# Kernel tuning notes

Hardware: AMD Instinct MI355X
Metric: run time of the kernel (lower is better)

The kernel has to match this reference:

```python
import jax, jax.numpy as jnp
import numpy as np

IN_FEATURES = 4096
OUT_FEATURES = 4096
SHARED_ROWS = 512
BATCH = 4096


def setup_inputs() -> dict:
    key = jax.random.key(0)
    k1, k2, k3 = jax.random.split(key, 3)
    x = jax.random.normal(k1, (BATCH, IN_FEATURES), dtype=jnp.float32)
    shared_weights = jax.random.normal(k2, (SHARED_ROWS, IN_FEATURES), dtype=jnp.float32)
    bias = jax.random.normal(k3, (OUT_FEATURES,), dtype=jnp.float32)
    return {"x": x, "shared_weights": shared_weights, "bias": bias}


def reference(x, shared_weights, bias):
    # Original: W = shared_weights.repeat(out_features // shared_rows, 1)  -> [out, in]
    #           y = x @ W.T + bias
    # Row i of W equals shared_weights[i % shared_rows], so the output columns are a
    # tile of the small GEMM result — compute the small GEMM once and tile (same math,
    # avoids materializing the full [out, in] weight).
    reps = OUT_FEATURES // SHARED_ROWS
    y_small = jnp.einsum("bi,ri->br", x, shared_weights)  # [batch, shared_rows]
    y = jnp.tile(y_small, (1, reps)) + bias  # [batch, out_features]
    return y
```

## Files before the change

### kernel.cpp

```cpp
#include <hip/hip_runtime.h>
#include <hip/hip_bf16.h>


typedef __bf16 bf8 __attribute__((ext_vector_type(8)));
typedef float f4 __attribute__((ext_vector_type(4)));
typedef unsigned int uint;

constexpr int M = 4096;
constexpr int K = 4096;
constexpr int NS = 512;
constexpr int OUTF = 4096;
constexpr int BM = 128, BN = 128, BK = 32;
constexpr int SK = 4;
constexpr int KS = K / SK;
constexpr int NITER = KS / BK;

#define PERM_HI2(hi, lo) __builtin_amdgcn_perm((hi), (lo), 0x07060302u)

__device__ __forceinline__ void async16(const float* g, float* l) {
  __builtin_amdgcn_global_load_lds(
      (const __attribute__((address_space(1))) void*)g,
      (__attribute__((address_space(3))) void*)l, 16, 0, 0);
}

__device__ __forceinline__ bf8 load_frag(const float* rowp, int q0) {
  const uint4* cp = reinterpret_cast<const uint4*>(rowp);
  uint4 lo = cp[q0];
  uint4 hi = cp[q0 ^ 1];
  uint4 f;
  f.x = PERM_HI2(lo.y, lo.x);
  f.y = PERM_HI2(lo.w, lo.z);
  f.z = PERM_HI2(hi.y, hi.x);
  f.w = PERM_HI2(hi.w, hi.z);
  return __builtin_bit_cast(bf8, f);
}

__global__ __launch_bounds__(256, 2)
void gemm_split_kernel(const float* __restrict__ x, const float* __restrict__ wgt,
                       float* __restrict__ out) {
  __shared__ __align__(16) float As[2][BM * BK];
  __shared__ __align__(16) float Bs[2][BN * BK];

  const int gid = blockIdx.x;
  const int mt = gid & 31;
  const int nt = (gid >> 5) & 3;
  const int s  = gid >> 7;

  const int tid  = threadIdx.x;
  const int wv   = tid >> 6;
  const int lane = tid & 63;

  int goff[4];
#pragma unroll
  for (int j = 0; j < 4; ++j) {
    const int c   = (wv * 4 + j) * 64 + lane;
    const int row = c >> 3;
    const int jg  = (c & 7) ^ (row & 7);
    goff[j] = row * K + jg * 4;
  }
  const int lbase = wv * 1024;

  const float* xT = x   + (size_t)(mt * BM) * K + s * KS;
  const float* wT = wgt + (size_t)(nt * BN) * K + s * KS;

  const int wm = (wv & 1) * 64;
  const int wn = (wv >> 1) * 64;
  const int lr = lane & 15;
  const int lq = lane >> 4;
  const int q0 = (2 * lq) ^ (lr & 7);

  f4 acc[4][4] = {};

#pragma unroll
  for (int j = 0; j < 4; ++j) {
    async16(xT + goff[j], &As[0][lbase + j * 256]);
    async16(wT + goff[j], &Bs[0][lbase + j * 256]);
  }
  __syncthreads();

  for (int kk = 0; kk < NITER; ++kk) {
    const int cur = kk & 1;

    if (kk + 1 < NITER) {
      const float* xn = xT + (kk + 1) * BK;
      const float* wn2 = wT + (kk + 1) * BK;
#pragma unroll
      for (int j = 0; j < 4; ++j) {
        async16(xn + goff[j],  &As[cur ^ 1][lbase + j * 256]);
        async16(wn2 + goff[j], &Bs[cur ^ 1][lbase + j * 256]);
      }
    }

    bf8 af[4], bfv[4];
#pragma unroll
    for (int mf = 0; mf < 4; ++mf)
      af[mf] = load_frag(&As[cur][(wm + mf * 16 + lr) * BK], q0);
#pragma unroll
    for (int nf = 0; nf < 4; ++nf)
      bfv[nf] = load_frag(&Bs[cur][(wn + nf * 16 + lr) * BK], q0);

#pragma unroll
    for (int mf = 0; mf < 4; ++mf)
#pragma unroll
      for (int nf = 0; nf < 4; ++nf)
        acc[mf][nf] = __builtin_amdgcn_mfma_f32_16x16x32_bf16(af[mf], bfv[nf], acc[mf][nf], 0, 0, 0);

    __syncthreads();
  }

  float* ob = out + (size_t)(mt * BM) * OUTF + s * NS + nt * BN;
#pragma unroll
  for (int mf = 0; mf < 4; ++mf) {
#pragma unroll
    for (int nf = 0; nf < 4; ++nf) {
#pragma unroll
      for (int r = 0; r < 4; ++r) {
        const int row = wm + mf * 16 + lq * 4 + r;
        const int col = wn + nf * 16 + lr;
        ob[(size_t)row * OUTF + col] = acc[mf][nf][r];
      }
    }
  }
}

__global__ __launch_bounds__(256)
void combine_kernel(float* __restrict__ out, const float* __restrict__ bias) {
  const int t = blockIdx.x * 256 + threadIdx.x;
  const int b  = t >> 7;
  const int rc = t & 127;
  float4* row = reinterpret_cast<float4*>(out) + (size_t)b * (OUTF / 4);
  const float4* bias4 = reinterpret_cast<const float4*>(bias);

  float4 p[SK];
#pragma unroll
  for (int s2 = 0; s2 < SK; ++s2) p[s2] = row[s2 * 128 + rc];

  float sx = 0.f, sy = 0.f, sz = 0.f, sw = 0.f;
#pragma unroll
  for (int s2 = 0; s2 < SK; ++s2) {
    sx += p[s2].x; sy += p[s2].y; sz += p[s2].z; sw += p[s2].w;
  }

#pragma unroll
  for (int c = 0; c < 8; ++c) {
    float4 bb = bias4[c * 128 + rc];
    float4 o;
    o.x = sx + bb.x; o.y = sy + bb.y; o.z = sz + bb.z; o.w = sw + bb.w;
    row[c * 128 + rc] = o;
  }
}

extern "C" void kernel_launch(void* const* d_in, const int* in_sizes, int n_in,
                              void* d_out, int out_size, void* d_ws, size_t ws_size,
                              hipStream_t stream) {
  (void)in_sizes; (void)n_in; (void)d_ws; (void)ws_size; (void)out_size;
  const float* x    = (const float*)d_in[0];
  const float* wgt  = (const float*)d_in[1];
  const float* bias = (const float*)d_in[2];
  float* out = (float*)d_out;

  gemm_split_kernel<<<dim3(32 * 4 * SK), dim3(256), 0, stream>>>(x, wgt, out);
  combine_kernel<<<dim3((M * NS / 4) / 256), dim3(256), 0, stream>>>(out, bias);
}
```

Baseline: 167.8 us.

## Pre-convert inputs to bf16, drop split-K, fuse bias and tiling into GEMM epilogue

Adds a pre-pass kernel that truncates x and the shared weights to bf16 in workspace, so the GEMM streams half the bytes and reads fragments straight from LDS without per-iteration repacking. Split-K and the separate combine kernel are removed. The GEMM now uses 64x64x64 tiles over the full K, with 512 blocks at higher occupancy, and writes all eight tiled output copies with bias added in the epilogue. The cost is an extra full pass over x (about 64MB read plus 32MB written), smaller tiles with less reuse per block, and uncoalesced scalar stores across eight column replicas.

```diff
diff --git a/kernel.cpp b/kernel.cpp
--- a/kernel.cpp
+++ b/kernel.cpp
@@ -5,76 +5,78 @@
 typedef __bf16 bf8 __attribute__((ext_vector_type(8)));
 typedef float f4 __attribute__((ext_vector_type(4)));
 typedef unsigned int uint;
+typedef unsigned short ushort;
 
 constexpr int M = 4096;
 constexpr int K = 4096;
 constexpr int NS = 512;
 constexpr int OUTF = 4096;
-constexpr int BM = 128, BN = 128, BK = 32;
-constexpr int SK = 4;
-constexpr int KS = K / SK;
-constexpr int NITER = KS / BK;
+constexpr int BM = 64, BN = 64, BK = 64;
+constexpr int NITER = K / BK;
 
 #define PERM_HI2(hi, lo) __builtin_amdgcn_perm((hi), (lo), 0x07060302u)
 
-__device__ __forceinline__ void async16(const float* g, float* l) {
+__device__ __forceinline__ void async16(const ushort* g, ushort* l) {
   __builtin_amdgcn_global_load_lds(
       (const __attribute__((address_space(1))) void*)g,
       (__attribute__((address_space(3))) void*)l, 16, 0, 0);
 }
 
-__device__ __forceinline__ bf8 load_frag(const float* rowp, int q0) {
-  const uint4* cp = reinterpret_cast<const uint4*>(rowp);
-  uint4 lo = cp[q0];
-  uint4 hi = cp[q0 ^ 1];
-  uint4 f;
-  f.x = PERM_HI2(lo.y, lo.x);
-  f.y = PERM_HI2(lo.w, lo.z);
-  f.z = PERM_HI2(hi.y, hi.x);
-  f.w = PERM_HI2(hi.w, hi.z);
-  return __builtin_bit_cast(bf8, f);
+__global__ __launch_bounds__(256)
+void convert_kernel(const float* __restrict__ x, const float* __restrict__ w,
+                    ushort* __restrict__ xb, ushort* __restrict__ wb) {
+  const size_t i = (size_t)blockIdx.x * 256 + threadIdx.x;
+  constexpr size_t NX = (size_t)M * K / 8;
+  const float* src;
+  ushort* dst;
+  if (i < NX) { src = x + i * 8; dst = xb + i * 8; }
+  else        { const size_t j = i - NX; src = w + j * 8; dst = wb + j * 8; }
+  const uint4 a = *reinterpret_cast<const uint4*>(src);
+  const uint4 b = *reinterpret_cast<const uint4*>(src + 4);
+  uint4 o;
+  o.x = PERM_HI2(a.y, a.x); o.y = PERM_HI2(a.w, a.z);
+  o.z = PERM_HI2(b.y, b.x); o.w = PERM_HI2(b.w, b.z);
+  *reinterpret_cast<uint4*>(dst) = o;
 }
 
-__global__ __launch_bounds__(256, 2)
-void gemm_split_kernel(const float* __restrict__ x, const float* __restrict__ wgt,
-                       float* __restrict__ out) {
-  __shared__ __align__(16) float As[2][BM * BK];
-  __shared__ __align__(16) float Bs[2][BN * BK];
+__global__ __launch_bounds__(256, 5)
+void gemm_kernel(const ushort* __restrict__ xb, const ushort* __restrict__ wb,
+                 const float* __restrict__ bias, float* __restrict__ out) {
+  __shared__ __align__(16) ushort As[2][BM * BK];
+  __shared__ __align__(16) ushort Bs[2][BN * BK];
 
   const int gid = blockIdx.x;
-  const int mt = gid & 31;
-  const int nt = (gid >> 5) & 3;
-  const int s  = gid >> 7;
+  const int nt = gid & 7;
+  const int mt = gid >> 3;
 
   const int tid  = threadIdx.x;
   const int wv   = tid >> 6;
   const int lane = tid & 63;
 
-  int goff[4];
+  int goff[2], lloc[2];
 #pragma unroll
-  for (int j = 0; j < 4; ++j) {
-    const int c   = (wv * 4 + j) * 64 + lane;
-    const int row = c >> 3;
-    const int jg  = (c & 7) ^ (row & 7);
-    goff[j] = row * K + jg * 4;
+  for (int j = 0; j < 2; ++j) {
+    const int c = (wv * 2 + j) * 64 + lane;
+    const int r = c >> 3;
+    const int g = (c & 7) ^ (r & 7);
+    goff[j] = r * K + g * 8;
+    lloc[j] = (wv * 2 + j) * 512;
   }
-  const int lbase = wv * 1024;
 
-  const float* xT = x   + (size_t)(mt * BM) * K + s * KS;
-  const float* wT = wgt + (size_t)(nt * BN) * K + s * KS;
+  const ushort* xT = xb + (size_t)(mt * BM) * K;
+  const ushort* wT = wb + (size_t)(nt * BN) * K;
 
-  const int wm = (wv & 1) * 64;
-  const int wn = (wv >> 1) * 64;
+  const int wm = (wv & 1) * 32;
+  const int wn = (wv >> 1) * 32;
   const int lr = lane & 15;
   const int lq = lane >> 4;
-  const int q0 = (2 * lq) ^ (lr & 7);
 
-  f4 acc[4][4] = {};
+  f4 acc[2][2] = {};
 
 #pragma unroll
-  for (int j = 0; j < 4; ++j) {
-    async16(xT + goff[j], &As[0][lbase + j * 256]);
-    async16(wT + goff[j], &Bs[0][lbase + j * 256]);
+  for (int j = 0; j < 2; ++j) {
+    async16(xT + goff[j], &As[0][lloc[j]]);
+    async16(wT + goff[j], &Bs[0][lloc[j]]);
   }
   __syncthreads();
 
@@ -82,83 +84,71 @@
     const int cur = kk & 1;
 
     if (kk + 1 < NITER) {
-      const float* xn = xT + (kk + 1) * BK;
-      const float* wn2 = wT + (kk + 1) * BK;
+      const int ko = (kk + 1) * BK;
 #pragma unroll
-      for (int j = 0; j < 4; ++j) {
-        async16(xn + goff[j],  &As[cur ^ 1][lbase + j * 256]);
-        async16(wn2 + goff[j], &Bs[cur ^ 1][lbase + j * 256]);
+      for (int j = 0; j < 2; ++j) {
+        async16(xT + ko + goff[j], &As[cur ^ 1][lloc[j]]);
+        async16(wT + ko + goff[j], &Bs[cur ^ 1][lloc[j]]);
       }
     }
 
-    bf8 af[4], bfv[4];
 #pragma unroll
-    for (int mf = 0; mf < 4; ++mf)
-      af[mf] = load_frag(&As[cur][(wm + mf * 16 + lr) * BK], q0);
+    for (int t = 0; t < 2; ++t) {
+      const int sc = ((t * 4 + lq) ^ (lr & 7)) * 8;
+      bf8 af[2], bfv[2];
 #pragma unroll
-    for (int nf = 0; nf < 4; ++nf)
-      bfv[nf] = load_frag(&Bs[cur][(wn + nf * 16 + lr) * BK], q0);
-
+      for (int mf = 0; mf < 2; ++mf)
+        af[mf] = *reinterpret_cast<const bf8*>(&As[cur][(wm + mf * 16 + lr) * BK + sc]);
 #pragma unroll
-    for (int mf = 0; mf < 4; ++mf)
+      for (int nf = 0; nf < 2; ++nf)
+        bfv[nf] = *reinterpret_cast<const bf8*>(&Bs[cur][(wn + nf * 16 + lr) * BK + sc]);
 #pragma unroll
-      for (int nf = 0; nf < 4; ++nf)
-        acc[mf][nf] = __builtin_amdgcn_mfma_f32_16x16x32_bf16(af[mf], bfv[nf], acc[mf][nf], 0, 0, 0);
+      for (int mf = 0; mf < 2; ++mf)
+#pragma unroll
+        for (int nf = 0; nf < 2; ++nf)
+          acc[mf][nf] = __builtin_amdgcn_mfma_f32_16x16x32_bf16(af[mf], bfv[nf], acc[mf][nf], 0, 0, 0);
+    }
 
     __syncthreads();
   }
 
-  float* ob = out + (size_t)(mt * BM) * OUTF + s * NS + nt * BN;
+  float bv[8][2];
 #pragma unroll
-  for (int mf = 0; mf < 4; ++mf) {
+  for (int rep = 0; rep < 8; ++rep)
 #pragma unroll
-    for (int nf = 0; nf < 4; ++nf) {
+    for (int nf = 0; nf < 2; ++nf)
+      bv[rep][nf] = bias[rep * NS + nt * BN + wn + nf * 16 + lr];
+
+  float* ob = out + (size_t)(mt * BM) * OUTF;
 #pragma unroll
-      for (int r = 0; r < 4; ++r) {
-        const int row = wm + mf * 16 + lq * 4 + r;
-        const int col = wn + nf * 16 + lr;
-        ob[(size_t)row * OUTF + col] = acc[mf][nf][r];
+  for (int mf = 0; mf < 2; ++mf)
+#pragma unroll
+    for (int r = 0; r < 4; ++r) {
+      const int row = wm + mf * 16 + lq * 4 + r;
+#pragma unroll
+      for (int nf = 0; nf < 2; ++nf) {
+        const float v = acc[mf][nf][r];
+        const int col0 = nt * BN + wn + nf * 16 + lr;
+#pragma unroll
+        for (int rep = 0; rep < 8; ++rep)
+          ob[(size_t)row * OUTF + rep * NS + col0] = v + bv[rep][nf];
       }
     }
-  }
-}
-
-__global__ __launch_bounds__(256)
-void combine_kernel(float* __restrict__ out, const float* __restrict__ bias) {
-  const int t = blockIdx.x * 256 + threadIdx.x;
-  const int b  = t >> 7;
-  const int rc = t & 127;
-  float4* row = reinterpret_cast<float4*>(out) + (size_t)b * (OUTF / 4);
-  const float4* bias4 = reinterpret_cast<const float4*>(bias);
-
-  float4 p[SK];
-#pragma unroll
-  for (int s2 = 0; s2 < SK; ++s2) p[s2] = row[s2 * 128 + rc];
-
-  float sx = 0.f, sy = 0.f, sz = 0.f, sw = 0.f;
-#pragma unroll
-  for (int s2 = 0; s2 < SK; ++s2) {
-    sx += p[s2].x; sy += p[s2].y; sz += p[s2].z; sw += p[s2].w;
-  }
-
-#pragma unroll
-  for (int c = 0; c < 8; ++c) {
-    float4 bb = bias4[c * 128 + rc];
-    float4 o;
-    o.x = sx + bb.x; o.y = sy + bb.y; o.z = sz + bb.z; o.w = sw + bb.w;
-    row[c * 128 + rc] = o;
-  }
 }
 
 extern "C" void kernel_launch(void* const* d_in, const int* in_sizes, int n_in,
                               void* d_out, int out_size, void* d_ws, size_t ws_size,
                               hipStream_t stream) {
-  (void)in_sizes; (void)n_in; (void)d_ws; (void)ws_size; (void)out_size;
+  (void)in_sizes; (void)n_in; (void)out_size; (void)ws_size;
   const float* x    = (const float*)d_in[0];
-  const float* wgt  = (const float*)d_in[1];
+  const float* w    = (const float*)d_in[1];
   const float* bias = (const float*)d_in[2];
   float* out = (float*)d_out;
 
-  gemm_split_kernel<<<dim3(32 * 4 * SK), dim3(256), 0, stream>>>(x, wgt, out);
-  combine_kernel<<<dim3((M * NS / 4) / 256), dim3(256), 0, stream>>>(out, bias);
+  ushort* xb = (ushort*)d_ws;
+  ushort* wb = (ushort*)d_ws + (size_t)M * K;
+
+  constexpr int conv_blocks = (int)(((size_t)M * K / 8 + (size_t)NS * K / 8) / 256);
+  convert_kernel<<<dim3(conv_blocks), dim3(256), 0, stream>>>(x, w, xb, wb);
+  gemm_kernel<<<dim3(64 * 8), dim3(256), 0, stream>>>(xb, wb, bias, out);
 }
```

New measurement: 170.8 us. No clear change (+1.8%).
